# Kernel optimization log

Hardware: AMD Instinct MI355X
Metric: run time of the kernel (lower is better)

## Reference

```python
import jax, jax.numpy as jnp
import numpy as np

D_MODEL = 768
HEAD_SIZE = 64

def setup_inputs() -> dict:
    key = jax.random.key(0)
    ks = jax.random.split(key, 7)
    B, S = 8, 2048
    x = jax.random.normal(ks[0], (B, S, D_MODEL), dtype=jnp.float32)
    s = 1.0 / np.sqrt(D_MODEL)
    Wq = jax.random.uniform(ks[1], (D_MODEL, HEAD_SIZE), jnp.float32, -s, s)
    bq = jnp.zeros((HEAD_SIZE,), jnp.float32)
    Wk = jax.random.uniform(ks[2], (D_MODEL, HEAD_SIZE), jnp.float32, -s, s)
    bk = jnp.zeros((HEAD_SIZE,), jnp.float32)
    Wv = jax.random.uniform(ks[3], (D_MODEL, HEAD_SIZE), jnp.float32, -s, s)
    bv = jnp.zeros((HEAD_SIZE,), jnp.float32)
    return {"x": x, "Wq": Wq, "bq": bq, "Wk": Wk, "bk": bk, "Wv": Wv, "bv": bv}

def reference(x, Wq, bq, Wk, bk, Wv, bv):
    # Single attention head: softmax(Q K^T / sqrt(head_size)) V
    q = jnp.einsum('bsd,dh->bsh', x, Wq) + bq  # [B,S,H]
    k = jnp.einsum('bsd,dh->bsh', x, Wk) + bk
    v = jnp.einsum('bsd,dh->bsh', x, Wv) + bv
    scale = 1.0 / jnp.sqrt(jnp.array(HEAD_SIZE, dtype=x.dtype))
    scores = jnp.einsum('bqh,bkh->bqk', q, k) * scale  # [B,S,S]
    attn = jax.nn.softmax(scores, axis=-1)
    out = jnp.einsum('bqk,bkh->bqh', attn, v)  # [B,S,H]
    return out
```

## Files before the change

### kernel.cpp

```cpp
#include <hip/hip_runtime.h>
#include <math.h>

#define D_MODEL 768
#define HS 64
#define BATCH 8
#define SEQ 2048
#define SCALE 0.125f

typedef _Float16 half_t;
typedef __attribute__((ext_vector_type(8))) _Float16 half8;
typedef __attribute__((ext_vector_type(4))) float floatx4;

__global__ __launch_bounds__(256)
void wconv_kernel(const float* __restrict__ Wq, const float* __restrict__ Wk,
                  const float* __restrict__ Wv, half_t* __restrict__ Wt)
{
    int m = blockIdx.x >> 6;
    int h = blockIdx.x & 63;
    const float* W = (m == 0) ? Wq : ((m == 1) ? Wk : Wv);
    half_t* dst = Wt + (size_t)blockIdx.x * D_MODEL;
    for (int k = threadIdx.x; k < D_MODEL; k += 256)
        dst[k] = (half_t)W[(size_t)k * HS + h];
}

__global__ __launch_bounds__(256)
void proj_kernel(const float* __restrict__ x, const half_t* __restrict__ Wt,
                 const float* __restrict__ bq, const float* __restrict__ bk,
                 const float* __restrict__ bv,
                 half_t* __restrict__ Qh, half_t* __restrict__ Kh,
                 half_t* __restrict__ Vt)
{
    __shared__ __align__(16) half_t xs[2][32 * 64];
    __shared__ __align__(16) half_t wt[2][192 * 64];

    const int tid = threadIdx.x;
    const int w = tid >> 6;
    const int lane = tid & 63;
    const int l15 = lane & 15;
    const int quad = lane >> 4;
    const long row0 = (long)blockIdx.x * 32;

    floatx4 acc[2][3];
#pragma unroll
    for (int i = 0; i < 2; ++i)
#pragma unroll
        for (int j = 0; j < 3; ++j) acc[i][j] = (floatx4){0.f, 0.f, 0.f, 0.f};

    const int xr = tid >> 3, xsc = tid & 7;
    const int xcg = xsc ^ (xr & 7);
    const float* xaddr = x + (row0 + xr) * D_MODEL + xcg * 8;

    float4 xA[2], xB[2];
    half8  wA[6], wB[6];

    auto loadx = [&](int k0, float4 (&v)[2]) {
        v[0] = *(const float4*)(xaddr + k0);
        v[1] = *(const float4*)(xaddr + k0 + 4);
    };
    auto loadw = [&](int k0, half8 (&wr)[6]) {
#pragma unroll
        for (int i = 0; i < 6; ++i) {
            int idx = i * 256 + tid;
            int r = idx >> 3, sc = idx & 7;
            int cg = sc ^ (r & 7);
            wr[i] = *(const half8*)(Wt + (size_t)r * D_MODEL + k0 + cg * 8);
        }
    };

    auto step = [&](int it, float4 (&xc)[2], half8 (&wc)[6],
                    float4 (&xn)[2], half8 (&wn)[6], int p) {
        half8 xh = (half8){(half_t)xc[0].x, (half_t)xc[0].y, (half_t)xc[0].z, (half_t)xc[0].w,
                           (half_t)xc[1].x, (half_t)xc[1].y, (half_t)xc[1].z, (half_t)xc[1].w};
        *(half8*)&xs[p][tid * 8] = xh;
#pragma unroll
        for (int i = 0; i < 6; ++i)
            *(half8*)&wt[p][(i * 256 + tid) * 8] = wc[i];
        __syncthreads();
        int kn = (it + 1 < 12) ? (it + 1) * 64 : 0;
        loadx(kn, xn);
        loadw(kn, wn);
#pragma unroll
        for (int kst = 0; kst < 2; ++kst) {
            half8 af[2];
#pragma unroll
            for (int mt = 0; mt < 2; ++mt) {
                int r = mt * 16 + l15;
                int slot = (kst * 4 + quad) ^ (r & 7);
                af[mt] = *(const half8*)&xs[p][r * 64 + slot * 8];
            }
#pragma unroll
            for (int nt = 0; nt < 3; ++nt) {
                int r = w * 48 + nt * 16 + l15;
                int slot = (kst * 4 + quad) ^ (r & 7);
                half8 bf = *(const half8*)&wt[p][r * 64 + slot * 8];
#pragma unroll
                for (int mt = 0; mt < 2; ++mt)
                    acc[mt][nt] = __builtin_amdgcn_mfma_f32_16x16x32_f16(
                        af[mt], bf, acc[mt][nt], 0, 0, 0);
            }
        }
    };

    loadx(0, xA);
    loadw(0, wA);
#pragma unroll
    for (int it = 0; it < 12; it += 2) {
        step(it,     xA, wA, xB, wB, 0);
        step(it + 1, xB, wB, xA, wA, 1);
    }

#pragma unroll
    for (int nt = 0; nt < 3; ++nt) {
        int nbase = w * 48 + nt * 16;
        int mm = nbase >> 6;
        int h = (nbase + l15) & 63;
        const float* bias = (mm == 0) ? bq : ((mm == 1) ? bk : bv);
        float bval = bias[h];
#pragma unroll
        for (int mt = 0; mt < 2; ++mt)
#pragma unroll
            for (int r = 0; r < 4; ++r) {
                long R = row0 + mt * 16 + quad * 4 + r;
                half_t hv = (half_t)(acc[mt][nt][r] + bval);
                if (mm == 0)      Qh[R * HS + h] = hv;
                else if (mm == 1) Kh[R * HS + h] = hv;
                else {
                    long b = R >> 11, s = R & 2047;
                    Vt[(b * HS + h) * SEQ + s] = hv;
                }
            }
    }
}

__global__ __launch_bounds__(256)
void attn_kernel(const half_t* __restrict__ Qh, const half_t* __restrict__ Kh,
                 const half_t* __restrict__ Vt,
                 half_t* __restrict__ Opart, float* __restrict__ lpart,
                 int kchunk)
{
    __shared__ __align__(16) half_t ks[2][64 * 64];
    __shared__ __align__(16) half_t vs[2][64 * 64];
    __shared__ __align__(16) half_t ps[4][32][72];

    const int tid = threadIdx.x;
    const int w = tid >> 6;
    const int lane = tid & 63;
    const int l15 = lane & 15;
    const int quad = lane >> 4;
    const int b = blockIdx.y;
    const int q0 = blockIdx.x * 256 + w * 64;
    const int kh = blockIdx.z;
    const int kk_begin = kh * kchunk;
    const int nk = kchunk >> 6;

    const half_t* Kb = Kh + (size_t)b * SEQ * HS;
    const half_t* Vb = Vt + (size_t)b * HS * SEQ;

    half8 qf[4][2];
#pragma unroll
    for (int mt = 0; mt < 4; ++mt)
#pragma unroll
        for (int kst = 0; kst < 2; ++kst) {
            half8 q = *(const half8*)(Qh + ((size_t)b * SEQ + q0 + mt * 16 + l15) * HS
                                      + kst * 32 + quad * 8);
#pragma unroll
            for (int j = 0; j < 8; ++j) q[j] = q[j] * (half_t)SCALE;
            qf[mt][kst] = q;
        }

    floatx4 oacc[4][4];
    float lsum[4][4];
#pragma unroll
    for (int mt = 0; mt < 4; ++mt) {
#pragma unroll
        for (int nt = 0; nt < 4; ++nt) oacc[mt][nt] = (floatx4){0.f, 0.f, 0.f, 0.f};
#pragma unroll
        for (int r = 0; r < 4; ++r) lsum[mt][r] = 0.f;
    }

    half8 kA[2], vA[2], kB[2], vB[2];

    auto loadkv = [&](int kk0, half8 (&kc)[2], half8 (&vc)[2]) {
#pragma unroll
        for (int i = 0; i < 2; ++i) {
            int idx = i * 256 + tid;
            int r = idx >> 3, sc = idx & 7;
            int cg = sc ^ (r & 7);
            kc[i] = *(const half8*)(Kb + (size_t)(kk0 + r) * HS + cg * 8);
            vc[i] = *(const half8*)(Vb + (size_t)r * SEQ + kk0 + cg * 8);
        }
    };

    auto step = [&](int kkn, half8 (&kc)[2], half8 (&vc)[2],
                    half8 (&kn_)[2], half8 (&vn_)[2], int p) {
#pragma unroll
        for (int i = 0; i < 2; ++i) {
            int idx = i * 256 + tid;
            *(half8*)&ks[p][idx * 8] = kc[i];
            *(half8*)&vs[p][idx * 8] = vc[i];
        }
        __syncthreads();
        loadkv(kkn, kn_, vn_);

        floatx4 sacc[4][4];
#pragma unroll
        for (int mt = 0; mt < 4; ++mt)
#pragma unroll
            for (int nt = 0; nt < 4; ++nt) sacc[mt][nt] = (floatx4){0.f, 0.f, 0.f, 0.f};
#pragma unroll
        for (int nt = 0; nt < 4; ++nt)
#pragma unroll
            for (int kst = 0; kst < 2; ++kst) {
                int r = nt * 16 + l15;
                int slot = (kst * 4 + quad) ^ (r & 7);
                half8 kf = *(const half8*)&ks[p][r * 64 + slot * 8];
#pragma unroll
                for (int mt = 0; mt < 4; ++mt)
                    sacc[mt][nt] = __builtin_amdgcn_mfma_f32_16x16x32_f16(
                        qf[mt][kst], kf, sacc[mt][nt], 0, 0, 0);
            }

#pragma unroll
        for (int h2 = 0; h2 < 2; ++h2) {
#pragma unroll
            for (int mtl = 0; mtl < 2; ++mtl) {
                int mt = h2 * 2 + mtl;
#pragma unroll
                for (int nt = 0; nt < 4; ++nt)
#pragma unroll
                    for (int r = 0; r < 4; ++r) {
                        float pv = __expf(sacc[mt][nt][r]);
                        lsum[mt][r] += pv;
                        ps[w][mtl * 16 + quad * 4 + r][nt * 16 + l15] = (half_t)pv;
                    }
            }
            half8 pfr[2][2];
#pragma unroll
            for (int mtl = 0; mtl < 2; ++mtl)
#pragma unroll
                for (int kst = 0; kst < 2; ++kst)
                    pfr[mtl][kst] = *(const half8*)&ps[w][mtl * 16 + l15][kst * 32 + quad * 8];
#pragma unroll
            for (int nt = 0; nt < 4; ++nt)
#pragma unroll
                for (int kst = 0; kst < 2; ++kst) {
                    int r = nt * 16 + l15;
                    int slot = (kst * 4 + quad) ^ (r & 7);
                    half8 vf = *(const half8*)&vs[p][r * 64 + slot * 8];
#pragma unroll
                    for (int mtl = 0; mtl < 2; ++mtl)
                        oacc[h2 * 2 + mtl][nt] = __builtin_amdgcn_mfma_f32_16x16x32_f16(
                            pfr[mtl][kst], vf, oacc[h2 * 2 + mtl][nt], 0, 0, 0);
                }
        }
    };

    loadkv(kk_begin, kA, vA);
    for (int it = 0; it < nk; it += 2) {
        int kk1 = kk_begin + it * 64 + 64;
        int kk2 = (it + 2 < nk) ? (kk1 + 64) : kk_begin;
        step(kk1, kA, vA, kB, vB, 0);
        step(kk2, kB, vB, kA, vA, 1);
    }

#pragma unroll
    for (int mt = 0; mt < 4; ++mt)
#pragma unroll
        for (int r = 0; r < 4; ++r) {
            float s = lsum[mt][r];
            s += __shfl_xor(s, 1);
            s += __shfl_xor(s, 2);
            s += __shfl_xor(s, 4);
            s += __shfl_xor(s, 8);
            lsum[mt][r] = s;
        }

    size_t obase = ((size_t)kh * BATCH + b) * SEQ * HS;
#pragma unroll
    for (int mt = 0; mt < 4; ++mt)
#pragma unroll
        for (int nt = 0; nt < 4; ++nt)
#pragma unroll
            for (int r = 0; r < 4; ++r) {
                int row = q0 + mt * 16 + quad * 4 + r;
                Opart[obase + (size_t)row * HS + nt * 16 + l15] = (half_t)oacc[mt][nt][r];
            }
    if (l15 == 0) {
#pragma unroll
        for (int mt = 0; mt < 4; ++mt)
#pragma unroll
            for (int r = 0; r < 4; ++r) {
                int row = q0 + mt * 16 + quad * 4 + r;
                lpart[((size_t)kh * BATCH + b) * SEQ + row] = lsum[mt][r];
            }
    }
}

__global__ __launch_bounds__(256)
void combine_kernel(const half_t* __restrict__ Opart, const float* __restrict__ lpart,
                    float* __restrict__ out, int nsplit)
{
    const size_t NT = (size_t)BATCH * SEQ * HS;
    const size_t BS = (size_t)BATCH * SEQ;
    size_t e0 = ((size_t)blockIdx.x * 256 + threadIdx.x) * 8;
    size_t row = e0 / HS;
    float o[8] = {0, 0, 0, 0, 0, 0, 0, 0};
    float l = 0.f;
    for (int i = 0; i < nsplit; ++i) {
        half8 oi = *(const half8*)(Opart + (size_t)i * NT + e0);
#pragma unroll
        for (int j = 0; j < 8; ++j) o[j] += (float)oi[j];
        l += lpart[(size_t)i * BS + row];
    }
    float inv = 1.f / l;
    float4 a = {o[0] * inv, o[1] * inv, o[2] * inv, o[3] * inv};
    float4 c = {o[4] * inv, o[5] * inv, o[6] * inv, o[7] * inv};
    *(float4*)(out + e0) = a;
    *(float4*)(out + e0 + 4) = c;
}

extern "C" void kernel_launch(void* const* d_in, const int* in_sizes, int n_in,
                              void* d_out, int out_size, void* d_ws, size_t ws_size,
                              hipStream_t stream) {
    const float* x  = (const float*)d_in[0];
    const float* Wq = (const float*)d_in[1];
    const float* bq = (const float*)d_in[2];
    const float* Wk = (const float*)d_in[3];
    const float* bk = (const float*)d_in[4];
    const float* Wv = (const float*)d_in[5];
    const float* bv = (const float*)d_in[6];
    float* out = (float*)d_out;

    const size_t per = (size_t)BATCH * SEQ * HS;
    half_t* Qh = (half_t*)d_ws;
    half_t* Kh = Qh + per;
    half_t* Vt = Kh + per;
    half_t* Wt = Vt + per;
    half_t* Opart = Wt + 3 * HS * D_MODEL;
    const size_t base_bytes = (3 * per + 3 * HS * D_MODEL) * sizeof(half_t);
    const size_t split_bytes = per * sizeof(half_t) + (size_t)BATCH * SEQ * sizeof(float);

    int ksplit = 2;
    if (ws_size >= base_bytes + 8 * split_bytes) ksplit = 8;
    else if (ws_size >= base_bytes + 4 * split_bytes) ksplit = 4;
    float* lpart = (float*)(Opart + (size_t)ksplit * per);

    wconv_kernel<<<dim3(3 * HS), dim3(256), 0, stream>>>(Wq, Wk, Wv, Wt);
    proj_kernel<<<dim3(BATCH * SEQ / 32), dim3(256), 0, stream>>>(
        x, Wt, bq, bk, bv, Qh, Kh, Vt);
    attn_kernel<<<dim3(SEQ / 256, BATCH, ksplit), dim3(256), 0, stream>>>(
        Qh, Kh, Vt, Opart, lpart, SEQ / ksplit);
    combine_kernel<<<dim3((BATCH * SEQ * HS) / (256 * 8)), dim3(256), 0, stream>>>(
        Opart, lpart, out, ksplit);
}
```

Baseline: 143.3 us.

## Fuse projection, attention and combine into one cooperative kernel with grid syncs

Merges the projection, split-K attention and combine stages into a single cooperative kernel of 512 blocks, separated by grid-wide barriers, to save launch gaps between kernels. Shared memory is single-buffered and shared through a union so two blocks can be resident per CU. Attention now computes scores in two halves to cut register pressure. The split factor is fixed at 8, and the old multi-kernel path remains as a fallback if the cooperative launch fails. In exchange it drops the register double-buffering, adds an extra barrier per iteration, and depends on all 512 blocks being co-resident.

```diff
diff --git a/kernel.cpp b/kernel.cpp
--- a/kernel.cpp
+++ b/kernel.cpp
@@ -1,4 +1,5 @@
 #include <hip/hip_runtime.h>
+#include <hip/hip_cooperative_groups.h>
 #include <math.h>
 
 #define D_MODEL 768
@@ -6,6 +7,10 @@
 #define BATCH 8
 #define SEQ 2048
 #define SCALE 0.125f
+#define KSPLIT 8
+#define KCHUNK (SEQ / KSPLIT)
+
+namespace cg = cooperative_groups;
 
 typedef _Float16 half_t;
 typedef __attribute__((ext_vector_type(8))) _Float16 half8;
@@ -23,6 +28,292 @@
         dst[k] = (half_t)W[(size_t)k * HS + h];
 }
 
+union SmemU {
+    struct {
+        half_t xs[32 * 64];
+        half_t wt[192 * 64];
+    } proj;
+    struct {
+        half_t ks[64 * 64];
+        half_t vs[64 * 64];
+        half_t ps[4][16][72];
+    } attn;
+};
+
+__global__ __launch_bounds__(256, 2)
+void fused_kernel(const float* __restrict__ x, const half_t* __restrict__ Wt,
+                  const float* __restrict__ bq, const float* __restrict__ bk,
+                  const float* __restrict__ bv,
+                  float* __restrict__ out,
+                  half_t* __restrict__ Qh, half_t* __restrict__ Kh,
+                  half_t* __restrict__ Vt,
+                  half_t* __restrict__ Opart, float* __restrict__ lpart)
+{
+    __shared__ SmemU sm;
+    cg::grid_group grid = cg::this_grid();
+
+    const int bid = blockIdx.x;
+    const int tid = threadIdx.x;
+    const int w = tid >> 6;
+    const int lane = tid & 63;
+    const int l15 = lane & 15;
+    const int quad = lane >> 4;
+
+    {
+        const long row0 = (long)bid * 32;
+
+        floatx4 acc[2][3];
+#pragma unroll
+        for (int i = 0; i < 2; ++i)
+#pragma unroll
+            for (int j = 0; j < 3; ++j) acc[i][j] = (floatx4){0.f, 0.f, 0.f, 0.f};
+
+        const int xr = tid >> 3, xsc = tid & 7;
+        const int xcg = xsc ^ (xr & 7);
+        const float* xaddr = x + (row0 + xr) * D_MODEL + xcg * 8;
+
+        float4 xc[2];
+        half8  wc[6];
+        auto loadx = [&](int k0) {
+            xc[0] = *(const float4*)(xaddr + k0);
+            xc[1] = *(const float4*)(xaddr + k0 + 4);
+        };
+        auto loadw = [&](int k0) {
+#pragma unroll
+            for (int i = 0; i < 6; ++i) {
+                int idx = i * 256 + tid;
+                int r = idx >> 3, sc = idx & 7;
+                int cg = sc ^ (r & 7);
+                wc[i] = *(const half8*)(Wt + (size_t)r * D_MODEL + k0 + cg * 8);
+            }
+        };
+
+        loadx(0);
+        loadw(0);
+        for (int it = 0; it < 12; ++it) {
+            half8 xh = (half8){(half_t)xc[0].x, (half_t)xc[0].y, (half_t)xc[0].z, (half_t)xc[0].w,
+                               (half_t)xc[1].x, (half_t)xc[1].y, (half_t)xc[1].z, (half_t)xc[1].w};
+            *(half8*)&sm.proj.xs[tid * 8] = xh;
+#pragma unroll
+            for (int i = 0; i < 6; ++i)
+                *(half8*)&sm.proj.wt[(i * 256 + tid) * 8] = wc[i];
+            __syncthreads();
+            int kn = (it + 1 < 12) ? (it + 1) * 64 : 0;
+            loadx(kn);
+            loadw(kn);
+#pragma unroll
+            for (int kst = 0; kst < 2; ++kst) {
+                half8 af[2];
+#pragma unroll
+                for (int mt = 0; mt < 2; ++mt) {
+                    int r = mt * 16 + l15;
+                    int slot = (kst * 4 + quad) ^ (r & 7);
+                    af[mt] = *(const half8*)&sm.proj.xs[r * 64 + slot * 8];
+                }
+#pragma unroll
+                for (int nt = 0; nt < 3; ++nt) {
+                    int r = w * 48 + nt * 16 + l15;
+                    int slot = (kst * 4 + quad) ^ (r & 7);
+                    half8 bf = *(const half8*)&sm.proj.wt[r * 64 + slot * 8];
+#pragma unroll
+                    for (int mt = 0; mt < 2; ++mt)
+                        acc[mt][nt] = __builtin_amdgcn_mfma_f32_16x16x32_f16(
+                            af[mt], bf, acc[mt][nt], 0, 0, 0);
+                }
+            }
+            __syncthreads();
+        }
+
+#pragma unroll
+        for (int nt = 0; nt < 3; ++nt) {
+            int nbase = w * 48 + nt * 16;
+            int mm = nbase >> 6;
+            int h = (nbase + l15) & 63;
+            const float* bias = (mm == 0) ? bq : ((mm == 1) ? bk : bv);
+            float bval = bias[h];
+#pragma unroll
+            for (int mt = 0; mt < 2; ++mt)
+#pragma unroll
+                for (int r = 0; r < 4; ++r) {
+                    long R = row0 + mt * 16 + quad * 4 + r;
+                    half_t hv = (half_t)(acc[mt][nt][r] + bval);
+                    if (mm == 0)      Qh[R * HS + h] = hv;
+                    else if (mm == 1) Kh[R * HS + h] = hv;
+                    else {
+                        long bb = R >> 11, s = R & 2047;
+                        Vt[(bb * HS + h) * SEQ + s] = hv;
+                    }
+                }
+        }
+    }
+
+    __threadfence();
+    grid.sync();
+
+    {
+        const int kh = bid >> 6;
+        const int b = (bid >> 3) & 7;
+        const int qblk = bid & 7;
+        const int q0 = qblk * 256 + w * 64;
+        const int kk_begin = kh * KCHUNK;
+
+        const half_t* Kb = Kh + (size_t)b * SEQ * HS;
+        const half_t* Vb = Vt + (size_t)b * HS * SEQ;
+
+        half8 qf[4][2];
+#pragma unroll
+        for (int mt = 0; mt < 4; ++mt)
+#pragma unroll
+            for (int kst = 0; kst < 2; ++kst) {
+                half8 q = *(const half8*)(Qh + ((size_t)b * SEQ + q0 + mt * 16 + l15) * HS
+                                          + kst * 32 + quad * 8);
+#pragma unroll
+                for (int j = 0; j < 8; ++j) q[j] = q[j] * (half_t)SCALE;
+                qf[mt][kst] = q;
+            }
+
+        floatx4 oacc[4][4];
+        float lsum[4][4];
+#pragma unroll
+        for (int mt = 0; mt < 4; ++mt) {
+#pragma unroll
+            for (int nt = 0; nt < 4; ++nt) oacc[mt][nt] = (floatx4){0.f, 0.f, 0.f, 0.f};
+#pragma unroll
+            for (int r = 0; r < 4; ++r) lsum[mt][r] = 0.f;
+        }
+
+        half8 kc[2], vc[2];
+        auto loadkv = [&](int kk0) {
+#pragma unroll
+            for (int i = 0; i < 2; ++i) {
+                int idx = i * 256 + tid;
+                int r = idx >> 3, sc = idx & 7;
+                int cg = sc ^ (r & 7);
+                kc[i] = *(const half8*)(Kb + (size_t)(kk0 + r) * HS + cg * 8);
+                vc[i] = *(const half8*)(Vb + (size_t)r * SEQ + kk0 + cg * 8);
+            }
+        };
+
+        loadkv(kk_begin);
+        for (int it = 0; it < KCHUNK / 64; ++it) {
+#pragma unroll
+            for (int i = 0; i < 2; ++i) {
+                int idx = i * 256 + tid;
+                *(half8*)&sm.attn.ks[idx * 8] = kc[i];
+                *(half8*)&sm.attn.vs[idx * 8] = vc[i];
+            }
+            __syncthreads();
+            int kkn = (it + 1 < KCHUNK / 64) ? kk_begin + (it + 1) * 64 : kk_begin;
+            loadkv(kkn);
+
+#pragma unroll
+            for (int h2 = 0; h2 < 2; ++h2) {
+                floatx4 sacc[2][4];
+#pragma unroll
+                for (int mtl = 0; mtl < 2; ++mtl)
+#pragma unroll
+                    for (int nt = 0; nt < 4; ++nt) sacc[mtl][nt] = (floatx4){0.f, 0.f, 0.f, 0.f};
+#pragma unroll
+                for (int nt = 0; nt < 4; ++nt)
+#pragma unroll
+                    for (int kst = 0; kst < 2; ++kst) {
+                        int r = nt * 16 + l15;
+                        int slot = (kst * 4 + quad) ^ (r & 7);
+                        half8 kf = *(const half8*)&sm.attn.ks[r * 64 + slot * 8];
+#pragma unroll
+                        for (int mtl = 0; mtl < 2; ++mtl)
+                            sacc[mtl][nt] = __builtin_amdgcn_mfma_f32_16x16x32_f16(
+                                qf[h2 * 2 + mtl][kst], kf, sacc[mtl][nt], 0, 0, 0);
+                    }
+
+#pragma unroll
+                for (int mtl = 0; mtl < 2; ++mtl) {
+                    int mt = h2 * 2 + mtl;
+#pragma unroll
+                    for (int nt = 0; nt < 4; ++nt)
+#pragma unroll
+                        for (int r = 0; r < 4; ++r) {
+                            float pv = __expf(sacc[mtl][nt][r]);
+                            lsum[mt][r] += pv;
+                            sm.attn.ps[w][quad * 4 + r][nt * 16 + l15] = (half_t)pv;
+                        }
+                    half8 pfr[2];
+#pragma unroll
+                    for (int kst = 0; kst < 2; ++kst)
+                        pfr[kst] = *(const half8*)&sm.attn.ps[w][l15][kst * 32 + quad * 8];
+#pragma unroll
+                    for (int nt = 0; nt < 4; ++nt)
+#pragma unroll
+                        for (int kst = 0; kst < 2; ++kst) {
+                            int r = nt * 16 + l15;
+                            int slot = (kst * 4 + quad) ^ (r & 7);
+                            half8 vf = *(const half8*)&sm.attn.vs[r * 64 + slot * 8];
+                            oacc[mt][nt] = __builtin_amdgcn_mfma_f32_16x16x32_f16(
+                                pfr[kst], vf, oacc[mt][nt], 0, 0, 0);
+                        }
+                }
+            }
+            __syncthreads();
+        }
+
+#pragma unroll
+        for (int mt = 0; mt < 4; ++mt)
+#pragma unroll
+            for (int r = 0; r < 4; ++r) {
+                float s = lsum[mt][r];
+                s += __shfl_xor(s, 1);
+                s += __shfl_xor(s, 2);
+                s += __shfl_xor(s, 4);
+                s += __shfl_xor(s, 8);
+                lsum[mt][r] = s;
+            }
+
+        size_t obase = ((size_t)kh * BATCH + b) * SEQ * HS;
+#pragma unroll
+        for (int mt = 0; mt < 4; ++mt)
+#pragma unroll
+            for (int nt = 0; nt < 4; ++nt)
+#pragma unroll
+                for (int r = 0; r < 4; ++r) {
+                    int row = q0 + mt * 16 + quad * 4 + r;
+                    Opart[obase + (size_t)row * HS + nt * 16 + l15] = (half_t)oacc[mt][nt][r];
+                }
+        if (l15 == 0) {
+#pragma unroll
+            for (int mt = 0; mt < 4; ++mt)
+#pragma unroll
+                for (int r = 0; r < 4; ++r) {
+                    int row = q0 + mt * 16 + quad * 4 + r;
+                    lpart[((size_t)kh * BATCH + b) * SEQ + row] = lsum[mt][r];
+                }
+        }
+    }
+
+    __threadfence();
+    grid.sync();
+
+    {
+        const size_t NT = (size_t)BATCH * SEQ * HS;
+        const size_t BS = (size_t)BATCH * SEQ;
+        size_t e0 = ((size_t)bid * 256 + tid) * 8;
+        size_t row = e0 / HS;
+        float o[8] = {0, 0, 0, 0, 0, 0, 0, 0};
+        float l = 0.f;
+#pragma unroll
+        for (int i = 0; i < KSPLIT; ++i) {
+            half8 oi = *(const half8*)(Opart + (size_t)i * NT + e0);
+#pragma unroll
+            for (int j = 0; j < 8; ++j) o[j] += (float)oi[j];
+            l += lpart[(size_t)i * BS + row];
+        }
+        float inv = 1.f / l;
+        float4 a = {o[0] * inv, o[1] * inv, o[2] * inv, o[3] * inv};
+        float4 c = {o[4] * inv, o[5] * inv, o[6] * inv, o[7] * inv};
+        *(float4*)(out + e0) = a;
+        *(float4*)(out + e0 + 4) = c;
+    }
+}
+
 __global__ __launch_bounds__(256)
 void proj_kernel(const float* __restrict__ x, const half_t* __restrict__ Wt,
                  const float* __restrict__ bq, const float* __restrict__ bk,
@@ -30,8 +321,8 @@
                  half_t* __restrict__ Qh, half_t* __restrict__ Kh,
                  half_t* __restrict__ Vt)
 {
-    __shared__ __align__(16) half_t xs[2][32 * 64];
-    __shared__ __align__(16) half_t wt[2][192 * 64];
+    __shared__ __align__(16) half_t xs[32 * 64];
+    __shared__ __align__(16) half_t wt[192 * 64];
 
     const int tid = threadIdx.x;
     const int w = tid >> 6;
@@ -50,35 +341,35 @@
     const int xcg = xsc ^ (xr & 7);
     const float* xaddr = x + (row0 + xr) * D_MODEL + xcg * 8;
 
-    float4 xA[2], xB[2];
-    half8  wA[6], wB[6];
-
-    auto loadx = [&](int k0, float4 (&v)[2]) {
-        v[0] = *(const float4*)(xaddr + k0);
-        v[1] = *(const float4*)(xaddr + k0 + 4);
+    float4 xc[2];
+    half8  wc[6];
+    auto loadx = [&](int k0) {
+        xc[0] = *(const float4*)(xaddr + k0);
+        xc[1] = *(const float4*)(xaddr + k0 + 4);
     };
-    auto loadw = [&](int k0, half8 (&wr)[6]) {
+    auto loadw = [&](int k0) {
 #pragma unroll
         for (int i = 0; i < 6; ++i) {
             int idx = i * 256 + tid;
             int r = idx >> 3, sc = idx & 7;
             int cg = sc ^ (r & 7);
-            wr[i] = *(const half8*)(Wt + (size_t)r * D_MODEL + k0 + cg * 8);
+            wc[i] = *(const half8*)(Wt + (size_t)r * D_MODEL + k0 + cg * 8);
         }
     };
 
-    auto step = [&](int it, float4 (&xc)[2], half8 (&wc)[6],
-                    float4 (&xn)[2], half8 (&wn)[6], int p) {
+    loadx(0);
+    loadw(0);
+    for (int it = 0; it < 12; ++it) {
         half8 xh = (half8){(half_t)xc[0].x, (half_t)xc[0].y, (half_t)xc[0].z, (half_t)xc[0].w,
                            (half_t)xc[1].x, (half_t)xc[1].y, (half_t)xc[1].z, (half_t)xc[1].w};
-        *(half8*)&xs[p][tid * 8] = xh;
+        *(half8*)&xs[tid * 8] = xh;
 #pragma unroll
         for (int i = 0; i < 6; ++i)
-            *(half8*)&wt[p][(i * 256 + tid) * 8] = wc[i];
+            *(half8*)&wt[(i * 256 + tid) * 8] = wc[i];
         __syncthreads();
         int kn = (it + 1 < 12) ? (it + 1) * 64 : 0;
-        loadx(kn, xn);
-        loadw(kn, wn);
+        loadx(kn);
+        loadw(kn);
 #pragma unroll
         for (int kst = 0; kst < 2; ++kst) {
             half8 af[2];
@@ -86,27 +377,20 @@
             for (int mt = 0; mt < 2; ++mt) {
                 int r = mt * 16 + l15;
                 int slot = (kst * 4 + quad) ^ (r & 7);
-                af[mt] = *(const half8*)&xs[p][r * 64 + slot * 8];
+                af[mt] = *(const half8*)&xs[r * 64 + slot * 8];
             }
 #pragma unroll
             for (int nt = 0; nt < 3; ++nt) {
                 int r = w * 48 + nt * 16 + l15;
                 int slot = (kst * 4 + quad) ^ (r & 7);
-                half8 bf = *(const half8*)&wt[p][r * 64 + slot * 8];
+                half8 bf = *(const half8*)&wt[r * 64 + slot * 8];
 #pragma unroll
                 for (int mt = 0; mt < 2; ++mt)
                     acc[mt][nt] = __builtin_amdgcn_mfma_f32_16x16x32_f16(
                         af[mt], bf, acc[mt][nt], 0, 0, 0);
             }
         }
-    };
-
-    loadx(0, xA);
-    loadw(0, wA);
-#pragma unroll
-    for (int it = 0; it < 12; it += 2) {
-        step(it,     xA, wA, xB, wB, 0);
-        step(it + 1, xB, wB, xA, wA, 1);
+        __syncthreads();
     }
 
 #pragma unroll
@@ -125,8 +409,8 @@
                 if (mm == 0)      Qh[R * HS + h] = hv;
                 else if (mm == 1) Kh[R * HS + h] = hv;
                 else {
-                    long b = R >> 11, s = R & 2047;
-                    Vt[(b * HS + h) * SEQ + s] = hv;
+                    long bb = R >> 11, s = R & 2047;
+                    Vt[(bb * HS + h) * SEQ + s] = hv;
                 }
             }
     }
@@ -138,9 +422,9 @@
                  half_t* __restrict__ Opart, float* __restrict__ lpart,
                  int kchunk)
 {
-    __shared__ __align__(16) half_t ks[2][64 * 64];
-    __shared__ __align__(16) half_t vs[2][64 * 64];
-    __shared__ __align__(16) half_t ps[4][32][72];
+    __shared__ __align__(16) half_t ks[64 * 64];
+    __shared__ __align__(16) half_t vs[64 * 64];
+    __shared__ __align__(16) half_t ps[4][16][72];
 
     const int tid = threadIdx.x;
     const int w = tid >> 6;
@@ -178,9 +462,8 @@
         for (int r = 0; r < 4; ++r) lsum[mt][r] = 0.f;
     }
 
-    half8 kA[2], vA[2], kB[2], vB[2];
-
-    auto loadkv = [&](int kk0, half8 (&kc)[2], half8 (&vc)[2]) {
+    half8 kc[2], vc[2];
+    auto loadkv = [&](int kk0) {
 #pragma unroll
         for (int i = 0; i < 2; ++i) {
             int idx = i * 256 + tid;
@@ -191,76 +474,66 @@
         }
     };
 
-    auto step = [&](int kkn, half8 (&kc)[2], half8 (&vc)[2],
-                    half8 (&kn_)[2], half8 (&vn_)[2], int p) {
+    loadkv(kk_begin);
+    for (int it = 0; it < nk; ++it) {
 #pragma unroll
         for (int i = 0; i < 2; ++i) {
             int idx = i * 256 + tid;
-            *(half8*)&ks[p][idx * 8] = kc[i];
-            *(half8*)&vs[p][idx * 8] = vc[i];
+            *(half8*)&ks[idx * 8] = kc[i];
+            *(half8*)&vs[idx * 8] = vc[i];
         }
         __syncthreads();
-        loadkv(kkn, kn_, vn_);
-
-        floatx4 sacc[4][4];
-#pragma unroll
-        for (int mt = 0; mt < 4; ++mt)
-#pragma unroll
-            for (int nt = 0; nt < 4; ++nt) sacc[mt][nt] = (floatx4){0.f, 0.f, 0.f, 0.f};
-#pragma unroll
-        for (int nt = 0; nt < 4; ++nt)
-#pragma unroll
-            for (int kst = 0; kst < 2; ++kst) {
-                int r = nt * 16 + l15;
-                int slot = (kst * 4 + quad) ^ (r & 7);
-                half8 kf = *(const half8*)&ks[p][r * 64 + slot * 8];
-#pragma unroll
-                for (int mt = 0; mt < 4; ++mt)
-                    sacc[mt][nt] = __builtin_amdgcn_mfma_f32_16x16x32_f16(
-                        qf[mt][kst], kf, sacc[mt][nt], 0, 0, 0);
-            }
+        int kkn = (it + 1 < nk) ? kk_begin + (it + 1) * 64 : kk_begin;
+        loadkv(kkn);
 
 #pragma unroll
         for (int h2 = 0; h2 < 2; ++h2) {
-#pragma unroll
-            for (int mtl = 0; mtl < 2; ++mtl) {
-                int mt = h2 * 2 + mtl;
-#pragma unroll
-                for (int nt = 0; nt < 4; ++nt)
-#pragma unroll
-                    for (int r = 0; r < 4; ++r) {
-                        float pv = __expf(sacc[mt][nt][r]);
-                        lsum[mt][r] += pv;
-                        ps[w][mtl * 16 + quad * 4 + r][nt * 16 + l15] = (half_t)pv;
-                    }
-            }
-            half8 pfr[2][2];
+            floatx4 sacc[2][4];
 #pragma unroll
             for (int mtl = 0; mtl < 2; ++mtl)
 #pragma unroll
-                for (int kst = 0; kst < 2; ++kst)
-                    pfr[mtl][kst] = *(const half8*)&ps[w][mtl * 16 + l15][kst * 32 + quad * 8];
+                for (int nt = 0; nt < 4; ++nt) sacc[mtl][nt] = (floatx4){0.f, 0.f, 0.f, 0.f};
 #pragma unroll
             for (int nt = 0; nt < 4; ++nt)
 #pragma unroll
                 for (int kst = 0; kst < 2; ++kst) {
                     int r = nt * 16 + l15;
                     int slot = (kst * 4 + quad) ^ (r & 7);
-                    half8 vf = *(const half8*)&vs[p][r * 64 + slot * 8];
+                    half8 kf = *(const half8*)&ks[r * 64 + slot * 8];
 #pragma unroll
                     for (int mtl = 0; mtl < 2; ++mtl)
-                        oacc[h2 * 2 + mtl][nt] = __builtin_amdgcn_mfma_f32_16x16x32_f16(
-                            pfr[mtl][kst], vf, oacc[h2 * 2 + mtl][nt], 0, 0, 0);
-                }
-        }
-    };
-
-    loadkv(kk_begin, kA, vA);
-    for (int it = 0; it < nk; it += 2) {
-        int kk1 = kk_begin + it * 64 + 64;
-        int kk2 = (it + 2 < nk) ? (kk1 + 64) : kk_begin;
-        step(kk1, kA, vA, kB, vB, 0);
-        step(kk2, kB, vB, kA, vA, 1);
+                        sacc[mtl][nt] = __builtin_amdgcn_mfma_f32_16x16x32_f16(
+                            qf[h2 * 2 + mtl][kst], kf, sacc[mtl][nt], 0, 0, 0);
+                }
+
+#pragma unroll
+            for (int mtl = 0; mtl < 2; ++mtl) {
+                int mt = h2 * 2 + mtl;
+#pragma unroll
+                for (int nt = 0; nt < 4; ++nt)
+#pragma unroll
+                    for (int r = 0; r < 4; ++r) {
+                        float pv = __expf(sacc[mtl][nt][r]);
+                        lsum[mt][r] += pv;
+                        ps[w][quad * 4 + r][nt * 16 + l15] = (half_t)pv;
+                    }
+                half8 pfr[2];
+#pragma unroll
+                for (int kst = 0; kst < 2; ++kst)
+                    pfr[kst] = *(const half8*)&ps[w][l15][kst * 32 + quad * 8];
+#pragma unroll
+                for (int nt = 0; nt < 4; ++nt)
+#pragma unroll
+                    for (int kst = 0; kst < 2; ++kst) {
+                        int r = nt * 16 + l15;
+                        int slot = (kst * 4 + quad) ^ (r & 7);
+                        half8 vf = *(const half8*)&vs[r * 64 + slot * 8];
+                        oacc[mt][nt] = __builtin_amdgcn_mfma_f32_16x16x32_f16(
+                            pfr[kst], vf, oacc[mt][nt], 0, 0, 0);
+                    }
+            }
+        }
+        __syncthreads();
     }
 
 #pragma unroll
@@ -337,19 +610,21 @@
     half_t* Vt = Kh + per;
     half_t* Wt = Vt + per;
     half_t* Opart = Wt + 3 * HS * D_MODEL;
-    const size_t base_bytes = (3 * per + 3 * HS * D_MODEL) * sizeof(half_t);
-    const size_t split_bytes = per * sizeof(half_t) + (size_t)BATCH * SEQ * sizeof(float);
-
-    int ksplit = 2;
-    if (ws_size >= base_bytes + 8 * split_bytes) ksplit = 8;
-    else if (ws_size >= base_bytes + 4 * split_bytes) ksplit = 4;
-    float* lpart = (float*)(Opart + (size_t)ksplit * per);
+    float*  lpart = (float*)(Opart + (size_t)KSPLIT * per);
 
     wconv_kernel<<<dim3(3 * HS), dim3(256), 0, stream>>>(Wq, Wk, Wv, Wt);
-    proj_kernel<<<dim3(BATCH * SEQ / 32), dim3(256), 0, stream>>>(
-        x, Wt, bq, bk, bv, Qh, Kh, Vt);
-    attn_kernel<<<dim3(SEQ / 256, BATCH, ksplit), dim3(256), 0, stream>>>(
-        Qh, Kh, Vt, Opart, lpart, SEQ / ksplit);
-    combine_kernel<<<dim3((BATCH * SEQ * HS) / (256 * 8)), dim3(256), 0, stream>>>(
-        Opart, lpart, out, ksplit);
+
+    void* args[] = {(void*)&x, (void*)&Wt, (void*)&bq, (void*)&bk, (void*)&bv,
+                    (void*)&out, (void*)&Qh, (void*)&Kh, (void*)&Vt,
+                    (void*)&Opart, (void*)&lpart};
+    hipError_t err = hipLaunchCooperativeKernel((void*)fused_kernel, dim3(512),
+                                                dim3(256), args, 0, stream);
+    if (err != hipSuccess) {
+        proj_kernel<<<dim3(BATCH * SEQ / 32), dim3(256), 0, stream>>>(
+            x, Wt, bq, bk, bv, Qh, Kh, Vt);
+        attn_kernel<<<dim3(SEQ / 256, BATCH, KSPLIT), dim3(256), 0, stream>>>(
+            Qh, Kh, Vt, Opart, lpart, KCHUNK);
+        combine_kernel<<<dim3((BATCH * SEQ * HS) / (256 * 8)), dim3(256), 0, stream>>>(
+            Opart, lpart, out, KSPLIT);
+    }
 }
```

After: 380.2 us. 2.65x slower.

## Load tiles straight into LDS with global_load_lds and fix split count

Applied to the files above, without the earlier changes.

Replaces register-staged, double-buffered global-to-LDS copies in the projection and attention kernels with direct global_load_lds transfers into single-buffered shared memory. Each tile is now waited on with a full waitcnt. The projection kernel stores x as fp32 in LDS and converts to fp16 at fragment read time. The attention kernel is restructured to process Q in two half-tiles with a smaller P scratch buffer and V fragments hoisted per tile. KSPLIT is fixed at 8 at compile time, which drops the workspace-size check. This cuts register pressure and LDS footprint to raise occupancy, but gives up the software prefetch overlap within each block.

```diff
diff --git a/kernel.cpp b/kernel.cpp
--- a/kernel.cpp
+++ b/kernel.cpp
@@ -6,10 +6,21 @@
 #define BATCH 8
 #define SEQ 2048
 #define SCALE 0.125f
+#define KSPLIT 8
+#define KCHUNK (SEQ / KSPLIT)
 
 typedef _Float16 half_t;
 typedef __attribute__((ext_vector_type(8))) _Float16 half8;
 typedef __attribute__((ext_vector_type(4))) float floatx4;
+
+typedef const __attribute__((address_space(1))) void gas_void;
+typedef __attribute__((address_space(3))) void las_void;
+__device__ __forceinline__ void gl_lds16(const void* g, void* l) {
+    __builtin_amdgcn_global_load_lds((gas_void*)g, (las_void*)l, 16, 0, 0);
+}
+__device__ __forceinline__ void waitcnt_all() {
+    __builtin_amdgcn_s_waitcnt(0);
+}
 
 __global__ __launch_bounds__(256)
 void wconv_kernel(const float* __restrict__ Wq, const float* __restrict__ Wk,
@@ -30,8 +41,8 @@
                  half_t* __restrict__ Qh, half_t* __restrict__ Kh,
                  half_t* __restrict__ Vt)
 {
-    __shared__ __align__(16) half_t xs[2][32 * 64];
-    __shared__ __align__(16) half_t wt[2][192 * 64];
+    __shared__ __align__(16) float  xs[32 * 64];
+    __shared__ __align__(16) half_t wt[192 * 64];
 
     const int tid = threadIdx.x;
     const int w = tid >> 6;
@@ -46,67 +57,48 @@
 #pragma unroll
         for (int j = 0; j < 3; ++j) acc[i][j] = (floatx4){0.f, 0.f, 0.f, 0.f};
 
-    const int xr = tid >> 3, xsc = tid & 7;
-    const int xcg = xsc ^ (xr & 7);
-    const float* xaddr = x + (row0 + xr) * D_MODEL + xcg * 8;
-
-    float4 xA[2], xB[2];
-    half8  wA[6], wB[6];
-
-    auto loadx = [&](int k0, float4 (&v)[2]) {
-        v[0] = *(const float4*)(xaddr + k0);
-        v[1] = *(const float4*)(xaddr + k0 + 4);
-    };
-    auto loadw = [&](int k0, half8 (&wr)[6]) {
+    for (int k0 = 0; k0 < D_MODEL; k0 += 64) {
+        __syncthreads();
+#pragma unroll
+        for (int i = 0; i < 2; ++i) {
+            int idx = i * 256 + tid;
+            int r = idx >> 4, sc = idx & 15;
+            int cg = sc ^ (r & 15);
+            gl_lds16(x + (row0 + r) * D_MODEL + k0 + cg * 4, xs + idx * 4);
+        }
 #pragma unroll
         for (int i = 0; i < 6; ++i) {
             int idx = i * 256 + tid;
             int r = idx >> 3, sc = idx & 7;
             int cg = sc ^ (r & 7);
-            wr[i] = *(const half8*)(Wt + (size_t)r * D_MODEL + k0 + cg * 8);
-        }
-    };
-
-    auto step = [&](int it, float4 (&xc)[2], half8 (&wc)[6],
-                    float4 (&xn)[2], half8 (&wn)[6], int p) {
-        half8 xh = (half8){(half_t)xc[0].x, (half_t)xc[0].y, (half_t)xc[0].z, (half_t)xc[0].w,
-                           (half_t)xc[1].x, (half_t)xc[1].y, (half_t)xc[1].z, (half_t)xc[1].w};
-        *(half8*)&xs[p][tid * 8] = xh;
-#pragma unroll
-        for (int i = 0; i < 6; ++i)
-            *(half8*)&wt[p][(i * 256 + tid) * 8] = wc[i];
+            gl_lds16(Wt + (size_t)r * D_MODEL + k0 + cg * 8, wt + idx * 8);
+        }
+        waitcnt_all();
         __syncthreads();
-        int kn = (it + 1 < 12) ? (it + 1) * 64 : 0;
-        loadx(kn, xn);
-        loadw(kn, wn);
+
 #pragma unroll
         for (int kst = 0; kst < 2; ++kst) {
             half8 af[2];
 #pragma unroll
             for (int mt = 0; mt < 2; ++mt) {
                 int r = mt * 16 + l15;
-                int slot = (kst * 4 + quad) ^ (r & 7);
-                af[mt] = *(const half8*)&xs[p][r * 64 + slot * 8];
+                int c0 = kst * 8 + quad * 2;
+                float4 f0 = *(const float4*)&xs[r * 64 + (c0 ^ l15) * 4];
+                float4 f1 = *(const float4*)&xs[r * 64 + ((c0 + 1) ^ l15) * 4];
+                af[mt] = (half8){(half_t)f0.x, (half_t)f0.y, (half_t)f0.z, (half_t)f0.w,
+                                 (half_t)f1.x, (half_t)f1.y, (half_t)f1.z, (half_t)f1.w};
             }
 #pragma unroll
             for (int nt = 0; nt < 3; ++nt) {
                 int r = w * 48 + nt * 16 + l15;
                 int slot = (kst * 4 + quad) ^ (r & 7);
-                half8 bf = *(const half8*)&wt[p][r * 64 + slot * 8];
+                half8 bf = *(const half8*)&wt[r * 64 + slot * 8];
 #pragma unroll
                 for (int mt = 0; mt < 2; ++mt)
                     acc[mt][nt] = __builtin_amdgcn_mfma_f32_16x16x32_f16(
                         af[mt], bf, acc[mt][nt], 0, 0, 0);
             }
         }
-    };
-
-    loadx(0, xA);
-    loadw(0, wA);
-#pragma unroll
-    for (int it = 0; it < 12; it += 2) {
-        step(it,     xA, wA, xB, wB, 0);
-        step(it + 1, xB, wB, xA, wA, 1);
     }
 
 #pragma unroll
@@ -125,8 +117,8 @@
                 if (mm == 0)      Qh[R * HS + h] = hv;
                 else if (mm == 1) Kh[R * HS + h] = hv;
                 else {
-                    long b = R >> 11, s = R & 2047;
-                    Vt[(b * HS + h) * SEQ + s] = hv;
+                    long bb = R >> 11, s = R & 2047;
+                    Vt[(bb * HS + h) * SEQ + s] = hv;
                 }
             }
     }
@@ -135,12 +127,11 @@
 __global__ __launch_bounds__(256)
 void attn_kernel(const half_t* __restrict__ Qh, const half_t* __restrict__ Kh,
                  const half_t* __restrict__ Vt,
-                 half_t* __restrict__ Opart, float* __restrict__ lpart,
-                 int kchunk)
+                 half_t* __restrict__ Opart, float* __restrict__ lpart)
 {
-    __shared__ __align__(16) half_t ks[2][64 * 64];
-    __shared__ __align__(16) half_t vs[2][64 * 64];
-    __shared__ __align__(16) half_t ps[4][32][72];
+    __shared__ __align__(16) half_t ks[64 * 64];
+    __shared__ __align__(16) half_t vs[64 * 64];
+    __shared__ __align__(16) half_t ps[4][16][72];
 
     const int tid = threadIdx.x;
     const int w = tid >> 6;
@@ -150,8 +141,7 @@
     const int b = blockIdx.y;
     const int q0 = blockIdx.x * 256 + w * 64;
     const int kh = blockIdx.z;
-    const int kk_begin = kh * kchunk;
-    const int nk = kchunk >> 6;
+    const int kk_begin = kh * KCHUNK;
 
     const half_t* Kb = Kh + (size_t)b * SEQ * HS;
     const half_t* Vb = Vt + (size_t)b * HS * SEQ;
@@ -178,89 +168,73 @@
         for (int r = 0; r < 4; ++r) lsum[mt][r] = 0.f;
     }
 
-    half8 kA[2], vA[2], kB[2], vB[2];
-
-    auto loadkv = [&](int kk0, half8 (&kc)[2], half8 (&vc)[2]) {
+    for (int it = 0; it < KCHUNK / 64; ++it) {
+        const int kk0 = kk_begin + it * 64;
+        __syncthreads();
 #pragma unroll
         for (int i = 0; i < 2; ++i) {
             int idx = i * 256 + tid;
             int r = idx >> 3, sc = idx & 7;
             int cg = sc ^ (r & 7);
-            kc[i] = *(const half8*)(Kb + (size_t)(kk0 + r) * HS + cg * 8);
-            vc[i] = *(const half8*)(Vb + (size_t)r * SEQ + kk0 + cg * 8);
-        }
-    };
-
-    auto step = [&](int kkn, half8 (&kc)[2], half8 (&vc)[2],
-                    half8 (&kn_)[2], half8 (&vn_)[2], int p) {
-#pragma unroll
-        for (int i = 0; i < 2; ++i) {
-            int idx = i * 256 + tid;
-            *(half8*)&ks[p][idx * 8] = kc[i];
-            *(half8*)&vs[p][idx * 8] = vc[i];
-        }
+            gl_lds16(Kb + (size_t)(kk0 + r) * HS + cg * 8, ks + idx * 8);
+            gl_lds16(Vb + (size_t)r * SEQ + kk0 + cg * 8, vs + idx * 8);
+        }
+        waitcnt_all();
         __syncthreads();
-        loadkv(kkn, kn_, vn_);
-
-        floatx4 sacc[4][4];
-#pragma unroll
-        for (int mt = 0; mt < 4; ++mt)
-#pragma unroll
-            for (int nt = 0; nt < 4; ++nt) sacc[mt][nt] = (floatx4){0.f, 0.f, 0.f, 0.f};
+
+        half8 vf[4][2];
 #pragma unroll
         for (int nt = 0; nt < 4; ++nt)
 #pragma unroll
             for (int kst = 0; kst < 2; ++kst) {
                 int r = nt * 16 + l15;
                 int slot = (kst * 4 + quad) ^ (r & 7);
-                half8 kf = *(const half8*)&ks[p][r * 64 + slot * 8];
-#pragma unroll
-                for (int mt = 0; mt < 4; ++mt)
-                    sacc[mt][nt] = __builtin_amdgcn_mfma_f32_16x16x32_f16(
-                        qf[mt][kst], kf, sacc[mt][nt], 0, 0, 0);
+                vf[nt][kst] = *(const half8*)&vs[r * 64 + slot * 8];
             }
 
 #pragma unroll
         for (int h2 = 0; h2 < 2; ++h2) {
-#pragma unroll
-            for (int mtl = 0; mtl < 2; ++mtl) {
-                int mt = h2 * 2 + mtl;
-#pragma unroll
-                for (int nt = 0; nt < 4; ++nt)
-#pragma unroll
-                    for (int r = 0; r < 4; ++r) {
-                        float pv = __expf(sacc[mt][nt][r]);
-                        lsum[mt][r] += pv;
-                        ps[w][mtl * 16 + quad * 4 + r][nt * 16 + l15] = (half_t)pv;
-                    }
-            }
-            half8 pfr[2][2];
+            floatx4 sacc[2][4];
 #pragma unroll
             for (int mtl = 0; mtl < 2; ++mtl)
 #pragma unroll
-                for (int kst = 0; kst < 2; ++kst)
-                    pfr[mtl][kst] = *(const half8*)&ps[w][mtl * 16 + l15][kst * 32 + quad * 8];
+                for (int nt = 0; nt < 4; ++nt) sacc[mtl][nt] = (floatx4){0.f, 0.f, 0.f, 0.f};
 #pragma unroll
             for (int nt = 0; nt < 4; ++nt)
 #pragma unroll
                 for (int kst = 0; kst < 2; ++kst) {
                     int r = nt * 16 + l15;
                     int slot = (kst * 4 + quad) ^ (r & 7);
-                    half8 vf = *(const half8*)&vs[p][r * 64 + slot * 8];
+                    half8 kf = *(const half8*)&ks[r * 64 + slot * 8];
 #pragma unroll
                     for (int mtl = 0; mtl < 2; ++mtl)
-                        oacc[h2 * 2 + mtl][nt] = __builtin_amdgcn_mfma_f32_16x16x32_f16(
-                            pfr[mtl][kst], vf, oacc[h2 * 2 + mtl][nt], 0, 0, 0);
+                        sacc[mtl][nt] = __builtin_amdgcn_mfma_f32_16x16x32_f16(
+                            qf[h2 * 2 + mtl][kst], kf, sacc[mtl][nt], 0, 0, 0);
                 }
-        }
-    };
-
-    loadkv(kk_begin, kA, vA);
-    for (int it = 0; it < nk; it += 2) {
-        int kk1 = kk_begin + it * 64 + 64;
-        int kk2 = (it + 2 < nk) ? (kk1 + 64) : kk_begin;
-        step(kk1, kA, vA, kB, vB, 0);
-        step(kk2, kB, vB, kA, vA, 1);
+
+#pragma unroll
+            for (int mtl = 0; mtl < 2; ++mtl) {
+                int mt = h2 * 2 + mtl;
+#pragma unroll
+                for (int nt = 0; nt < 4; ++nt)
+#pragma unroll
+                    for (int r = 0; r < 4; ++r) {
+                        float pv = __expf(sacc[mtl][nt][r]);
+                        lsum[mt][r] += pv;
+                        ps[w][quad * 4 + r][nt * 16 + l15] = (half_t)pv;
+                    }
+                half8 pfr[2];
+#pragma unroll
+                for (int kst = 0; kst < 2; ++kst)
+                    pfr[kst] = *(const half8*)&ps[w][l15][kst * 32 + quad * 8];
+#pragma unroll
+                for (int nt = 0; nt < 4; ++nt)
+#pragma unroll
+                    for (int kst = 0; kst < 2; ++kst)
+                        oacc[mt][nt] = __builtin_amdgcn_mfma_f32_16x16x32_f16(
+                            pfr[kst], vf[nt][kst], oacc[mt][nt], 0, 0, 0);
+            }
+        }
     }
 
 #pragma unroll
@@ -298,7 +272,7 @@
 
 __global__ __launch_bounds__(256)
 void combine_kernel(const half_t* __restrict__ Opart, const float* __restrict__ lpart,
-                    float* __restrict__ out, int nsplit)
+                    float* __restrict__ out)
 {
     const size_t NT = (size_t)BATCH * SEQ * HS;
     const size_t BS = (size_t)BATCH * SEQ;
@@ -306,7 +280,8 @@
     size_t row = e0 / HS;
     float o[8] = {0, 0, 0, 0, 0, 0, 0, 0};
     float l = 0.f;
-    for (int i = 0; i < nsplit; ++i) {
+#pragma unroll
+    for (int i = 0; i < KSPLIT; ++i) {
         half8 oi = *(const half8*)(Opart + (size_t)i * NT + e0);
 #pragma unroll
         for (int j = 0; j < 8; ++j) o[j] += (float)oi[j];
@@ -337,19 +312,13 @@
     half_t* Vt = Kh + per;
     half_t* Wt = Vt + per;
     half_t* Opart = Wt + 3 * HS * D_MODEL;
-    const size_t base_bytes = (3 * per + 3 * HS * D_MODEL) * sizeof(half_t);
-    const size_t split_bytes = per * sizeof(half_t) + (size_t)BATCH * SEQ * sizeof(float);
-
-    int ksplit = 2;
-    if (ws_size >= base_bytes + 8 * split_bytes) ksplit = 8;
-    else if (ws_size >= base_bytes + 4 * split_bytes) ksplit = 4;
-    float* lpart = (float*)(Opart + (size_t)ksplit * per);
+    float*  lpart = (float*)(Opart + (size_t)KSPLIT * per);
 
     wconv_kernel<<<dim3(3 * HS), dim3(256), 0, stream>>>(Wq, Wk, Wv, Wt);
     proj_kernel<<<dim3(BATCH * SEQ / 32), dim3(256), 0, stream>>>(
         x, Wt, bq, bk, bv, Qh, Kh, Vt);
-    attn_kernel<<<dim3(SEQ / 256, BATCH, ksplit), dim3(256), 0, stream>>>(
-        Qh, Kh, Vt, Opart, lpart, SEQ / ksplit);
+    attn_kernel<<<dim3(SEQ / 256, BATCH, KSPLIT), dim3(256), 0, stream>>>(
+        Qh, Kh, Vt, Opart, lpart);
     combine_kernel<<<dim3((BATCH * SEQ * HS) / (256 * 8)), dim3(256), 0, stream>>>(
-        Opart, lpart, out, ksplit);
-}
+        Opart, lpart, out);
+}
```

Measured after the change: 141.8 us. Within noise of the previous version (-1.1%).
